# Optimization experiments

Measured on AMD Instinct MI355X. Metric: run time of the kernel, lower is better.

Reference implementation:

```python
import jax, jax.numpy as jnp
import numpy as np
from jax import lax

B, M = 16384, 128
NUM_LAYERS, OW, OH = 22, 11, 11
MAX_VEC = np.array([9.0, 1.0, 1.0, 10.0, 3.0, 254.0, 1.0, 1.0, 235.0, 8.0, 9.0, 250.0,
                    29.0, 1.0, 1.0, 8.0, 1.0, 1.0, 6.0, 3.0, 1.0, 2.0], dtype=np.float32)


def setup_inputs() -> dict:
    key = jax.random.key(0)
    ks = jax.random.split(key, 20)
    s = 0.05
    return {
        "observations": jax.random.randint(ks[0], (B, M, 3), 0, 255, dtype=jnp.int32),
        "cnn1_w": jax.random.normal(ks[1], (64, 22, 5, 5), jnp.float32) * s,
        "cnn1_b": jnp.zeros((64,), jnp.float32),
        "cnn2_w": jax.random.normal(ks[2], (64, 64, 3, 3), jnp.float32) * s,
        "cnn2_b": jnp.zeros((64,), jnp.float32),
        "fc1_w": jax.random.normal(ks[3], (128, 64), jnp.float32) * s,
        "fc1_b": jnp.zeros((128,), jnp.float32),
        "enc_w": jax.random.normal(ks[4], (128, 128), jnp.float32) * s,
        "enc_b": jnp.zeros((128,), jnp.float32),
        "critic1_w": jax.random.normal(ks[5], (1024, 128), jnp.float32) * s,
        "critic1_b": jnp.zeros((1024,), jnp.float32),
        "value_w": jax.random.normal(ks[6], (1, 1024), jnp.float32) * s,
        "value_b": jnp.zeros((1,), jnp.float32),
        "actor1_w": jax.random.normal(ks[7], (512, 128), jnp.float32) * s,
        "actor1_b": jnp.zeros((512,), jnp.float32),
        "action_emb": jax.random.normal(ks[8], (100, 16), jnp.float32) * s,
        "head0_w": jax.random.normal(ks[9], (9, 528), jnp.float32) * s,
        "head0_b": jnp.zeros((9,), jnp.float32),
        "head1_w": jax.random.normal(ks[10], (10, 528), jnp.float32) * s,
        "head1_b": jnp.zeros((10,), jnp.float32),
    }


def _encode_scatter(observations):
    # zero-out any byte equal to 255 (matches torch in-place masking)
    tok = jnp.where(observations == 255, 0, observations)  # [B, M, 3]
    coords = tok[..., 0].astype(jnp.uint8)
    x = ((coords >> 4) & 15).astype(jnp.int32)
    y = (coords & 15).astype(jnp.int32)
    atr = tok[..., 1].astype(jnp.int32)
    val = tok[..., 2].astype(jnp.float32)
    b, m = atr.shape
    valid = (x < OW) & (y < OH) & (atr < NUM_LAYERS)
    b_idx = jnp.broadcast_to(jnp.arange(b, dtype=jnp.int32)[:, None], (b, m))
    b_idx = jnp.where(valid, b_idx, b)  # route invalid tokens out of bounds -> dropped
    box = jnp.zeros((b, NUM_LAYERS, OW, OH), jnp.float32)
    box = box.at[b_idx, atr, x, y].set(val, mode="drop")
    return box


def _forward(observations, cnn1_w, cnn1_b, cnn2_w, cnn2_b, fc1_w, fc1_b, enc_w, enc_b,
             critic1_w, critic1_b, value_w, value_b, actor1_w, actor1_b, action_emb,
             head0_w, head0_b, head1_w, head1_b):
    box = _encode_scatter(observations)
    x = box / jnp.asarray(MAX_VEC)[None, :, None, None]
    dn = ("NCHW", "OIHW", "NCHW")
    x = lax.conv_general_dilated(x, cnn1_w, (3, 3), "VALID", dimension_numbers=dn) + cnn1_b[None, :, None, None]
    x = lax.conv_general_dilated(x, cnn2_w, (1, 1), "VALID", dimension_numbers=dn) + cnn2_b[None, :, None, None]
    x = x.reshape(x.shape[0], -1)                 # [B, 64]
    x = x @ fc1_w.T + fc1_b                       # [B, 128]
    hidden = x @ enc_w.T + enc_b                  # [B, 128]
    critic = jnp.tanh(hidden @ critic1_w.T + critic1_b)
    value = critic @ value_w.T + value_b          # [B, 1]
    actor = hidden @ actor1_w.T + actor1_b        # [B, 512]
    emb = jnp.broadcast_to(action_emb.mean(axis=0)[None, :], (actor.shape[0], action_emb.shape[1]))
    comb = jnp.concatenate([actor, emb], axis=-1)  # [B, 528]
    logits = jnp.concatenate([comb @ head0_w.T + head0_b, comb @ head1_w.T + head1_b], axis=-1)
    return logits, value


def reference(observations, cnn1_w, cnn1_b, cnn2_w, cnn2_b, fc1_w, fc1_b, enc_w, enc_b,
              critic1_w, critic1_b, value_w, value_b, actor1_w, actor1_b, action_emb,
              head0_w, head0_b, head1_w, head1_b):
    return _forward(observations, cnn1_w, cnn1_b, cnn2_w, cnn2_b, fc1_w, fc1_b, enc_w, enc_b,
                    critic1_w, critic1_b, value_w, value_b, actor1_w, actor1_b, action_emb,
                    head0_w, head0_b, head1_w, head1_b)
```

## Files before the change

kernel.cpp:

```cpp
#include <hip/hip_runtime.h>
#include <math.h>

#define NB 16384
#define NTOK 128
#define NKEY 2662
#define NLOG 19
#define TB 16

typedef __attribute__((ext_vector_type(8))) short short8;
typedef __attribute__((ext_vector_type(4))) float floatx4;

__device__ __constant__ float c_maxv[22] = {
    9.f, 1.f, 1.f, 10.f, 3.f, 254.f, 1.f, 1.f, 235.f, 8.f, 9.f, 250.f,
    29.f, 1.f, 1.f, 8.f, 1.f, 1.f, 6.f, 3.f, 1.f, 2.f};

__device__ __forceinline__ unsigned short f2bf(float f) {
    unsigned u = __float_as_uint(f);
    return (unsigned short)((u + 0x7FFFu + ((u >> 16) & 1u)) >> 16);
}
__device__ __forceinline__ float tanh_fast(float x) {
    float e = __builtin_amdgcn_exp2f(x * 2.885390082f);
    return 1.f - 2.f * __builtin_amdgcn_rcpf(e + 1.f);
}

__global__ __launch_bounds__(256) void k_pre1(
    const float* __restrict__ w1, const float* __restrict__ b1,
    const float* __restrict__ w2, const float* __restrict__ b2,
    const float* __restrict__ fc1w, const float* __restrict__ encw,
    const float* __restrict__ h0w, const float* __restrict__ h1w,
    const float* __restrict__ a1w, const float* __restrict__ aemb,
    const float* __restrict__ c1w,
    float* __restrict__ G, float* __restrict__ E,
    float* __restrict__ h2b, float* __restrict__ emb,
    float* __restrict__ Wlog, unsigned short* __restrict__ c1wb)
{
    __shared__ float s_w2[72 * 65];
    const int bid = blockIdx.x, t = threadIdx.x;
    if (bid < 666) {
        const int v = t & 63;
        const int key_u = __builtin_amdgcn_readfirstlane(bid * 4 + (t >> 6));
        const int key_c = (key_u < NKEY) ? key_u : (NKEY - 1);
        const int c = key_c / 121, rem = key_c % 121, X = rem / 11, Y = rem % 11;
        float acc = 0.f;
        for (int u0 = 0; u0 < 64; u0 += 8) {
            __syncthreads();
            #pragma unroll
            for (int r = 0; r < 18; ++r) {
                int g = t + 256 * r;
                int vg = g / 72, rg = g % 72;
                s_w2[rg * 65 + vg] = w2[vg * 576 + u0 * 9 + rg];
            }
            __syncthreads();
            #pragma unroll
            for (int ur = 0; ur < 8; ++ur) {
                const int w1base = (u0 + ur) * 550 + c * 25;
                #pragma unroll
                for (int i = 0; i < 3; ++i) {
                    int xi = X - 3 * i;
                    if (xi < 0 || xi > 4) continue;
                    #pragma unroll
                    for (int j = 0; j < 3; ++j) {
                        int yj = Y - 3 * j;
                        if (yj < 0 || yj > 4) continue;
                        acc += s_w2[(ur * 9 + i * 3 + j) * 65 + v] *
                               w1[w1base + xi * 5 + yj];
                    }
                }
            }
        }
        if (key_u < NKEY) G[key_u * 64 + v] = acc;
    } else if (bid < 698) {
        int m = (bid - 666) * 256 + t;
        int h = __builtin_amdgcn_readfirstlane(m >> 6) & 127;
        int v = t & 63;
        float acc = 0.f;
        #pragma unroll 8
        for (int p = 0; p < 128; ++p)
            acc += encw[h * 128 + p] * fc1w[p * 64 + v];
        E[v * 128 + h] = acc;
    } else if (bid == 698) {
        if (t < 64) {
            float s = b2[t];
            for (int u = 0; u < 64; ++u) {
                float ws = 0.f;
                for (int k = 0; k < 9; ++k) ws += w2[(t * 64 + u) * 9 + k];
                s += b1[u] * ws;
            }
            h2b[t] = s;
        } else if (t < 80) {
            int e = t - 64;
            float s = 0.f;
            for (int r = 0; r < 100; ++r) s += aemb[r * 16 + e];
            emb[e] = s * 0.01f;
        }
    } else if (bid < 709) {
        int n = (bid - 699) * 256 + t;
        if (n < NLOG * 128) {
            int o = __builtin_amdgcn_readfirstlane(n >> 7);
            int h = n & 127;
            const float* hw = (o < 9) ? (h0w + o * 528) : (h1w + (o - 9) * 528);
            float acc = 0.f;
            #pragma unroll 8
            for (int a = 0; a < 512; ++a)
                acc += hw[a] * a1w[a * 128 + h];
            Wlog[n] = acc;
        }
    } else {
        int n = (bid - 709) * 256 + t;
        c1wb[n] = f2bf(c1w[n]);
    }
}

__global__ __launch_bounds__(256) void k_pre2(
    const float* __restrict__ G, const float* __restrict__ E,
    const float* __restrict__ h2b, const float* __restrict__ emb,
    const float* __restrict__ fc1w, const float* __restrict__ fc1b,
    const float* __restrict__ encw, const float* __restrict__ encb,
    const float* __restrict__ a1b,
    const float* __restrict__ h0w, const float* __restrict__ h0b,
    const float* __restrict__ h1w, const float* __restrict__ h1b,
    float* __restrict__ Weff, float* __restrict__ beff, float* __restrict__ blog)
{
    const int bid = blockIdx.x, t = threadIdx.x;
    if (bid < 1331) {
        int n = bid * 256 + t;
        int key = __builtin_amdgcn_readfirstlane(n >> 7);
        int h = n & 127;
        float acc = 0.f;
        #pragma unroll 8
        for (int v = 0; v < 64; ++v)
            acc += E[v * 128 + h] * G[key * 64 + v];
        Weff[n] = acc / c_maxv[key / 121];
    } else {
        __shared__ float s_t[128];
        if (t < 128) {
            float s = fc1b[t];
            for (int v = 0; v < 64; ++v) s += fc1w[t * 64 + v] * h2b[v];
            s_t[t] = s;
        }
        __syncthreads();
        if (t < 128) {
            float s = encb[t];
            for (int p = 0; p < 128; ++p) s += encw[t * 128 + p] * s_t[p];
            beff[t] = s;
        } else if (t < 128 + NLOG) {
            int o = t - 128;
            float s = (o < 9) ? h0b[o] : h1b[o - 9];
            for (int a = 0; a < 512; ++a) {
                float hw = (o < 9) ? h0w[o * 528 + a] : h1w[(o - 9) * 528 + a];
                s += hw * a1b[a];
            }
            for (int e = 0; e < 16; ++e) {
                float hw = (o < 9) ? h0w[o * 528 + 512 + e] : h1w[(o - 9) * 528 + 512 + e];
                s += hw * emb[e];
            }
            blog[o] = s;
        }
    }
}

__global__ __launch_bounds__(256) void k_main(
    const int* __restrict__ obs,
    const float* __restrict__ Weff, const float* __restrict__ beff,
    const unsigned short* __restrict__ c1wb, const float* __restrict__ c1b,
    const float* __restrict__ vw, const float* __restrict__ vb,
    const float* __restrict__ Wlog, const float* __restrict__ blog,
    float* __restrict__ out)
{
    __shared__ int            s_lst[TB * 32];
    __shared__ float          s_hidden[TB * 128];
    __shared__ unsigned short s_hb[TB * 136];
    __shared__ int            s_cnt[TB];
    __shared__ float          s_val[64];

    const int tid = threadIdx.x, bid = blockIdx.x;
    const int b0 = bid * TB;

    if (tid < TB) s_cnt[tid] = 0;
    __syncthreads();

    {
        const int gtok0 = b0 * NTOK;
        #pragma unroll
        for (int k = 0; k < TB * NTOK / 256; ++k) {
            int tt = tid + 256 * k;
            int gi = (gtok0 + tt) * 3;
            int o0 = obs[gi], o1 = obs[gi + 1], o2 = obs[gi + 2];
            o0 = (o0 == 255) ? 0 : o0;
            o1 = (o1 == 255) ? 0 : o1;
            o2 = (o2 == 255) ? 0 : o2;
            int x = (o0 >> 4) & 15, y = o0 & 15;
            if (x < 11 && y < 11 && o1 < 22) {
                int bb = tt >> 7, m = tt & 127;
                int pos = atomicAdd(&s_cnt[bb], 1);
                if (pos < 32)
                    s_lst[bb * 32 + pos] = (m << 20) | (o2 << 12) | (o1 * 121 + x * 11 + y);
            }
        }
    }
    __syncthreads();

    {
        int bb = tid >> 4, e0 = tid & 15;
        int n = s_cnt[bb]; if (n > 32) n = 32;
        #pragma unroll
        for (int r = 0; r < 2; ++r) {
            int e = e0 + 16 * r;
            if (e < n) {
                int p = s_lst[bb * 32 + e];
                bool dead = false;
                for (int i = 0; i < n; ++i) {
                    int q = s_lst[bb * 32 + i];
                    dead |= (((q ^ p) & 0xFFF) == 0) && (q > p);
                }
                if (dead) s_lst[bb * 32 + e] = p & ~0x000FF000;
            }
        }
    }
    __syncthreads();

    {
        int h = tid & 127, bg = tid >> 7;
        for (int bb = bg; bb < TB; bb += 2) {
            float acc = beff[h];
            int n = s_cnt[bb]; if (n > 32) n = 32;
            for (int i = 0; i < n; ++i) {
                int p = s_lst[bb * 32 + i];
                acc += (float)((p >> 12) & 0xFF) * Weff[(p & 0xFFF) * 128 + h];
            }
            s_hidden[bb * 128 + h] = acc;
            s_hb[bb * 136 + h] = f2bf(acc);
        }
    }
    __syncthreads();

    {
        const int lane = tid & 63, w = tid >> 6;
        const int lm = lane & 15, quad = lane >> 4;
        short8 af[4];
        #pragma unroll
        for (int kk = 0; kk < 4; ++kk)
            af[kk] = *(const short8*)&s_hb[lm * 136 + kk * 32 + quad * 8];

        float vpart[4] = {0.f, 0.f, 0.f, 0.f};
        for (int nt = 0; nt < 16; ++nt) {
            int j = w * 256 + nt * 16 + lm;
            floatx4 acc = {0.f, 0.f, 0.f, 0.f};
            #pragma unroll
            for (int kk = 0; kk < 4; ++kk) {
                short8 bf = *(const short8*)&c1wb[j * 128 + kk * 32 + quad * 8];
                acc = __builtin_amdgcn_mfma_f32_16x16x32_bf16(af[kk], bf, acc, 0, 0, 0);
            }
            float bj = c1b[j], wj = vw[j];
            #pragma unroll
            for (int r = 0; r < 4; ++r)
                vpart[r] += tanh_fast(acc[r] + bj) * wj;
        }
        #pragma unroll
        for (int off = 1; off <= 8; off <<= 1)
            #pragma unroll
            for (int r = 0; r < 4; ++r)
                vpart[r] += __shfl_xor(vpart[r], off, 64);
        if (lm == 0) {
            #pragma unroll
            for (int r = 0; r < 4; ++r)
                s_val[w * 16 + quad * 4 + r] = vpart[r];
        }
    }
    __syncthreads();
    if (tid < TB) {
        float v = s_val[tid] + s_val[16 + tid] + s_val[32 + tid] + s_val[48 + tid];
        out[NB * NLOG + b0 + tid] = v + vb[0];
    }

    {
        const float4* s_h4 = (const float4*)s_hidden;
        const float4* wl4  = (const float4*)Wlog;
        int bl = tid >> 4, oo = tid & 15;
        #pragma unroll
        for (int rep = 0; rep < 2; ++rep) {
            int o = oo + rep * 16;
            if (o < NLOG) {
                float acc = blog[o];
                #pragma unroll
                for (int hq = 0; hq < 32; ++hq) {
                    float4 hv = s_h4[bl * 32 + hq];
                    float4 wl = wl4[o * 32 + hq];
                    acc += wl.x * hv.x + wl.y * hv.y + wl.z * hv.z + wl.w * hv.w;
                }
                out[(b0 + bl) * NLOG + o] = acc;
            }
        }
    }
}

extern "C" void kernel_launch(void* const* d_in, const int* in_sizes, int n_in,
                              void* d_out, int out_size, void* d_ws, size_t ws_size,
                              hipStream_t stream)
{
    const int*   obs  = (const int*)  d_in[0];
    const float* w1   = (const float*)d_in[1];
    const float* b1   = (const float*)d_in[2];
    const float* w2   = (const float*)d_in[3];
    const float* b2   = (const float*)d_in[4];
    const float* fc1w = (const float*)d_in[5];
    const float* fc1b = (const float*)d_in[6];
    const float* encw = (const float*)d_in[7];
    const float* encb = (const float*)d_in[8];
    const float* c1w  = (const float*)d_in[9];
    const float* c1b  = (const float*)d_in[10];
    const float* vw   = (const float*)d_in[11];
    const float* vb   = (const float*)d_in[12];
    const float* a1w  = (const float*)d_in[13];
    const float* a1b  = (const float*)d_in[14];
    const float* aemb = (const float*)d_in[15];
    const float* h0w  = (const float*)d_in[16];
    const float* h0b  = (const float*)d_in[17];
    const float* h1w  = (const float*)d_in[18];
    const float* h1b  = (const float*)d_in[19];

    float* W    = (float*)d_ws;
    float* G    = W;
    float* E    = W + 170368;
    float* h2b  = W + 178560;
    float* emb  = W + 178624;
    float* Weff = W + 178640;
    float* beff = W + 519376;
    float* Wlog = W + 519504;
    float* blog = W + 521936;
    unsigned short* c1wb = (unsigned short*)(W + 524288);

    hipLaunchKernelGGL(k_pre1, dim3(1221), dim3(256), 0, stream,
                       w1, b1, w2, b2, fc1w, encw, h0w, h1w, a1w, aemb, c1w,
                       G, E, h2b, emb, Wlog, c1wb);
    hipLaunchKernelGGL(k_pre2, dim3(1332), dim3(256), 0, stream,
                       G, E, h2b, emb, fc1w, fc1b, encw, encb, a1b,
                       h0w, h0b, h1w, h1b, Weff, beff, blog);
    hipLaunchKernelGGL(k_main, dim3(NB / TB), dim3(256), 0, stream,
                       obs, Weff, beff, c1wb, c1b, vw, vb, Wlog, blog,
                       (float*)d_out);
}
```

Before: 210.3 us.

## Double main-kernel batch tile, vectorize loads, and restructure precompute reductions

The main kernel now handles 32 samples per block with 512 threads. Each c1 weight fragment is reused for two MFMA row tiles, observations are read as int4 vectors, and the gather loop for two samples is interleaved to raise memory-level parallelism. The precompute kernels prefetch w2 into registers ahead of the shared-memory store, change the E layout to allow float4 dot products, and split serial reductions (h2b, emb, blog) across threads with shuffles. These changes touch several independent parts and increase per-thread register pressure in exchange for fewer blocks and less redundant weight traffic.

```diff
diff --git a/kernel.cpp b/kernel.cpp
--- a/kernel.cpp
+++ b/kernel.cpp
@@ -5,7 +5,7 @@
 #define NTOK 128
 #define NKEY 2662
 #define NLOG 19
-#define TB 16
+#define TB 32
 
 typedef __attribute__((ext_vector_type(8))) short short8;
 typedef __attribute__((ext_vector_type(4))) float floatx4;
@@ -41,16 +41,43 @@
         const int key_u = __builtin_amdgcn_readfirstlane(bid * 4 + (t >> 6));
         const int key_c = (key_u < NKEY) ? key_u : (NKEY - 1);
         const int c = key_c / 121, rem = key_c % 121, X = rem / 11, Y = rem % 11;
+
+        const int vg0 = t / 72, rg0 = t - vg0 * 72;
+        const int base0 = vg0 * 576 + rg0;
+
+        float rw[18];
+        {
+            int rg = rg0, base = base0;
+            #pragma unroll
+            for (int r = 0; r < 18; ++r) {
+                rw[r] = w2[base];
+                rg += 40; base += 1768;
+                if (rg >= 72) { rg -= 72; base += 504; }
+            }
+        }
         float acc = 0.f;
-        for (int u0 = 0; u0 < 64; u0 += 8) {
+        for (int s = 0; s < 8; ++s) {
             __syncthreads();
-            #pragma unroll
-            for (int r = 0; r < 18; ++r) {
-                int g = t + 256 * r;
-                int vg = g / 72, rg = g % 72;
-                s_w2[rg * 65 + vg] = w2[vg * 576 + u0 * 9 + rg];
+            {
+                int rg = rg0, vg = vg0;
+                #pragma unroll
+                for (int r = 0; r < 18; ++r) {
+                    s_w2[rg * 65 + vg] = rw[r];
+                    rg += 40; vg += 3;
+                    if (rg >= 72) { rg -= 72; vg += 1; }
+                }
             }
             __syncthreads();
+            if (s < 7) {
+                int rg = rg0, base = base0 + (s + 1) * 72;
+                #pragma unroll
+                for (int r = 0; r < 18; ++r) {
+                    rw[r] = w2[base];
+                    rg += 40; base += 1768;
+                    if (rg >= 72) { rg -= 72; base += 504; }
+                }
+            }
+            const int u0 = s * 8;
             #pragma unroll
             for (int ur = 0; ur < 8; ++ur) {
                 const int w1base = (u0 + ur) * 550 + c * 25;
@@ -77,24 +104,33 @@
         #pragma unroll 8
         for (int p = 0; p < 128; ++p)
             acc += encw[h * 128 + p] * fc1w[p * 64 + v];
-        E[v * 128 + h] = acc;
+        E[h * 64 + v] = acc;
     } else if (bid == 698) {
+        int o = t >> 2, q = t & 3;
+        const float* wp = w2 + (o * 64 + q * 16) * 9;
+        float s = 0.f;
+        #pragma unroll
+        for (int ui = 0; ui < 16; ++ui) {
+            float ws = 0.f;
+            #pragma unroll
+            for (int k = 0; k < 9; ++k) ws += wp[ui * 9 + k];
+            s += b1[q * 16 + ui] * ws;
+        }
+        s += __shfl_xor(s, 1, 64);
+        s += __shfl_xor(s, 2, 64);
+        if (q == 0) h2b[o] = s + b2[o];
+    } else if (bid == 699) {
         if (t < 64) {
-            float s = b2[t];
-            for (int u = 0; u < 64; ++u) {
-                float ws = 0.f;
-                for (int k = 0; k < 9; ++k) ws += w2[(t * 64 + u) * 9 + k];
-                s += b1[u] * ws;
-            }
-            h2b[t] = s;
-        } else if (t < 80) {
-            int e = t - 64;
+            int e = t & 15, rq = t >> 4;
             float s = 0.f;
-            for (int r = 0; r < 100; ++r) s += aemb[r * 16 + e];
-            emb[e] = s * 0.01f;
-        }
-    } else if (bid < 709) {
-        int n = (bid - 699) * 256 + t;
+            #pragma unroll
+            for (int rr = 0; rr < 25; ++rr) s += aemb[(rq * 25 + rr) * 16 + e];
+            s += __shfl_xor(s, 16, 64);
+            s += __shfl_xor(s, 32, 64);
+            if (t < 16) emb[e] = s * 0.01f;
+        }
+    } else if (bid < 710) {
+        int n = (bid - 700) * 256 + t;
         if (n < NLOG * 128) {
             int o = __builtin_amdgcn_readfirstlane(n >> 7);
             int h = n & 127;
@@ -106,7 +142,7 @@
             Wlog[n] = acc;
         }
     } else {
-        int n = (bid - 709) * 256 + t;
+        int n = (bid - 710) * 256 + t;
         c1wb[n] = f2bf(c1w[n]);
     }
 }
@@ -121,45 +157,73 @@
     const float* __restrict__ h1w, const float* __restrict__ h1b,
     float* __restrict__ Weff, float* __restrict__ beff, float* __restrict__ blog)
 {
+    __shared__ float s_h2[64];
+    __shared__ float s_t[128];
     const int bid = blockIdx.x, t = threadIdx.x;
     if (bid < 1331) {
         int n = bid * 256 + t;
         int key = __builtin_amdgcn_readfirstlane(n >> 7);
         int h = n & 127;
+        const float4* E4 = (const float4*)E;
+        const float4* G4 = (const float4*)(G + key * 64);
         float acc = 0.f;
-        #pragma unroll 8
-        for (int v = 0; v < 64; ++v)
-            acc += E[v * 128 + h] * G[key * 64 + v];
+        #pragma unroll
+        for (int vq = 0; vq < 16; ++vq) {
+            float4 e = E4[h * 16 + vq];
+            float4 g = G4[vq];
+            acc += e.x * g.x + e.y * g.y + e.z * g.z + e.w * g.w;
+        }
         Weff[n] = acc / c_maxv[key / 121];
     } else {
-        __shared__ float s_t[128];
-        if (t < 128) {
-            float s = fc1b[t];
-            for (int v = 0; v < 64; ++v) s += fc1w[t * 64 + v] * h2b[v];
-            s_t[t] = s;
-        }
+        if (t < 64) s_h2[t] = h2b[t];
         __syncthreads();
         if (t < 128) {
+            const float4* f4 = (const float4*)(fc1w + t * 64);
+            float s = fc1b[t];
+            #pragma unroll
+            for (int vq = 0; vq < 16; ++vq) {
+                float4 w = f4[vq];
+                s += w.x * s_h2[vq * 4]     + w.y * s_h2[vq * 4 + 1] +
+                     w.z * s_h2[vq * 4 + 2] + w.w * s_h2[vq * 4 + 3];
+            }
+            s_t[t] = s;
+        } else {
+            int tp = t - 128;
+            int os = tp >> 3, ai = tp & 7;
+            #pragma unroll
+            for (int rep = 0; rep < 2; ++rep) {
+                int o = os + rep * 16;
+                int oc = (o < NLOG) ? o : (NLOG - 1);
+                const float* hw = (oc < 9) ? (h0w + oc * 528)
+                                           : (h1w + (oc - 9) * 528);
+                float s = 0.f;
+                for (int a = ai; a < 528; a += 8) {
+                    float m = (a < 512) ? a1b[a] : emb[a - 512];
+                    s += hw[a] * m;
+                }
+                s += __shfl_xor(s, 1, 64);
+                s += __shfl_xor(s, 2, 64);
+                s += __shfl_xor(s, 4, 64);
+                if (ai == 0 && o < NLOG)
+                    blog[o] = s + ((o < 9) ? h0b[o] : h1b[o - 9]);
+            }
+        }
+        __syncthreads();
+        if (t < 128) {
+            const float4* e4 = (const float4*)(encw + t * 128);
             float s = encb[t];
-            for (int p = 0; p < 128; ++p) s += encw[t * 128 + p] * s_t[p];
+            #pragma unroll
+            for (int pq = 0; pq < 32; ++pq) {
+                float4 w = e4[pq];
+                s += w.x * s_t[pq * 4]     + w.y * s_t[pq * 4 + 1] +
+                     w.z * s_t[pq * 4 + 2] + w.w * s_t[pq * 4 + 3];
+            }
             beff[t] = s;
-        } else if (t < 128 + NLOG) {
-            int o = t - 128;
-            float s = (o < 9) ? h0b[o] : h1b[o - 9];
-            for (int a = 0; a < 512; ++a) {
-                float hw = (o < 9) ? h0w[o * 528 + a] : h1w[(o - 9) * 528 + a];
-                s += hw * a1b[a];
-            }
-            for (int e = 0; e < 16; ++e) {
-                float hw = (o < 9) ? h0w[o * 528 + 512 + e] : h1w[(o - 9) * 528 + 512 + e];
-                s += hw * emb[e];
-            }
-            blog[o] = s;
-        }
-    }
-}
-
-__global__ __launch_bounds__(256) void k_main(
+        }
+    }
+}
+
+__global__ __launch_bounds__(512, 4) void k_main(
     const int* __restrict__ obs,
     const float* __restrict__ Weff, const float* __restrict__ beff,
     const unsigned short* __restrict__ c1wb, const float* __restrict__ c1b,
@@ -171,7 +235,7 @@
     __shared__ float          s_hidden[TB * 128];
     __shared__ unsigned short s_hb[TB * 136];
     __shared__ int            s_cnt[TB];
-    __shared__ float          s_val[64];
+    __shared__ float          s_val[8 * 32];
 
     const int tid = threadIdx.x, bid = blockIdx.x;
     const int b0 = bid * TB;
@@ -182,19 +246,27 @@
     {
         const int gtok0 = b0 * NTOK;
         #pragma unroll
-        for (int k = 0; k < TB * NTOK / 256; ++k) {
-            int tt = tid + 256 * k;
-            int gi = (gtok0 + tt) * 3;
-            int o0 = obs[gi], o1 = obs[gi + 1], o2 = obs[gi + 2];
-            o0 = (o0 == 255) ? 0 : o0;
-            o1 = (o1 == 255) ? 0 : o1;
-            o2 = (o2 == 255) ? 0 : o2;
-            int x = (o0 >> 4) & 15, y = o0 & 15;
-            if (x < 11 && y < 11 && o1 < 22) {
-                int bb = tt >> 7, m = tt & 127;
-                int pos = atomicAdd(&s_cnt[bb], 1);
-                if (pos < 32)
-                    s_lst[bb * 32 + pos] = (m << 20) | (o2 << 12) | (o1 * 121 + x * 11 + y);
+        for (int k = 0; k < TB * NTOK / (512 * 4); ++k) {
+            int g = tid + 512 * k;
+            const int4* p = (const int4*)(obs + (size_t)(gtok0 + 4 * g) * 3);
+            int4 A = p[0], Bv = p[1], Cv = p[2];
+            int d[12] = {A.x, A.y, A.z, A.w, Bv.x, Bv.y, Bv.z, Bv.w,
+                         Cv.x, Cv.y, Cv.z, Cv.w};
+            #pragma unroll
+            for (int s = 0; s < 4; ++s) {
+                int o0 = d[3 * s], o1 = d[3 * s + 1], o2 = d[3 * s + 2];
+                o0 = (o0 == 255) ? 0 : o0;
+                o1 = (o1 == 255) ? 0 : o1;
+                o2 = (o2 == 255) ? 0 : o2;
+                int x = (o0 >> 4) & 15, y = o0 & 15;
+                if (x < 11 && y < 11 && o1 < 22) {
+                    int tt = 4 * g + s;
+                    int bb = tt >> 7, m = tt & 127;
+                    int pos = atomicAdd(&s_cnt[bb], 1);
+                    if (pos < 32)
+                        s_lst[bb * 32 + pos] =
+                            (m << 20) | (o2 << 12) | (o1 * 121 + x * 11 + y);
+                }
             }
         }
     }
@@ -221,15 +293,26 @@
 
     {
         int h = tid & 127, bg = tid >> 7;
-        for (int bb = bg; bb < TB; bb += 2) {
-            float acc = beff[h];
-            int n = s_cnt[bb]; if (n > 32) n = 32;
-            for (int i = 0; i < n; ++i) {
-                int p = s_lst[bb * 32 + i];
-                acc += (float)((p >> 12) & 0xFF) * Weff[(p & 0xFFF) * 128 + h];
-            }
-            s_hidden[bb * 128 + h] = acc;
-            s_hb[bb * 136 + h] = f2bf(acc);
+        float be = beff[h];
+        #pragma unroll
+        for (int it = 0; it < 4; ++it) {
+            int bbA = bg + it * 8, bbB = bbA + 4;
+            int nA = s_cnt[bbA]; if (nA > 32) nA = 32;
+            int nB = s_cnt[bbB]; if (nB > 32) nB = 32;
+            int nm = (nA > nB) ? nA : nB;
+            float aA = be, aB = be;
+            for (int i = 0; i < nm; ++i) {
+                if (i < nA) {
+                    int p = s_lst[bbA * 32 + i];
+                    aA += (float)((p >> 12) & 0xFF) * Weff[(p & 0xFFF) * 128 + h];
+                }
+                if (i < nB) {
+                    int p = s_lst[bbB * 32 + i];
+                    aB += (float)((p >> 12) & 0xFF) * Weff[(p & 0xFFF) * 128 + h];
+                }
+            }
+            s_hidden[bbA * 128 + h] = aA; s_hb[bbA * 136 + h] = f2bf(aA);
+            s_hidden[bbB * 128 + h] = aB; s_hb[bbB * 136 + h] = f2bf(aB);
         }
     }
     __syncthreads();
@@ -237,39 +320,51 @@
     {
         const int lane = tid & 63, w = tid >> 6;
         const int lm = lane & 15, quad = lane >> 4;
-        short8 af[4];
-        #pragma unroll
-        for (int kk = 0; kk < 4; ++kk)
-            af[kk] = *(const short8*)&s_hb[lm * 136 + kk * 32 + quad * 8];
-
-        float vpart[4] = {0.f, 0.f, 0.f, 0.f};
-        for (int nt = 0; nt < 16; ++nt) {
-            int j = w * 256 + nt * 16 + lm;
-            floatx4 acc = {0.f, 0.f, 0.f, 0.f};
+        short8 af0[4], af1[4];
+        #pragma unroll
+        for (int kk = 0; kk < 4; ++kk) {
+            af0[kk] = *(const short8*)&s_hb[lm * 136 + kk * 32 + quad * 8];
+            af1[kk] = *(const short8*)&s_hb[(16 + lm) * 136 + kk * 32 + quad * 8];
+        }
+        float vp0[4] = {0.f, 0.f, 0.f, 0.f}, vp1[4] = {0.f, 0.f, 0.f, 0.f};
+        for (int nt = 0; nt < 8; ++nt) {
+            int j = w * 128 + nt * 16 + lm;
+            const short8* cp = (const short8*)&c1wb[j * 128];
+            floatx4 a0 = {0.f, 0.f, 0.f, 0.f}, a1 = {0.f, 0.f, 0.f, 0.f};
             #pragma unroll
             for (int kk = 0; kk < 4; ++kk) {
-                short8 bf = *(const short8*)&c1wb[j * 128 + kk * 32 + quad * 8];
-                acc = __builtin_amdgcn_mfma_f32_16x16x32_bf16(af[kk], bf, acc, 0, 0, 0);
+                short8 bf = cp[kk * 4 + quad];
+                a0 = __builtin_amdgcn_mfma_f32_16x16x32_bf16(af0[kk], bf, a0, 0, 0, 0);
+                a1 = __builtin_amdgcn_mfma_f32_16x16x32_bf16(af1[kk], bf, a1, 0, 0, 0);
             }
             float bj = c1b[j], wj = vw[j];
             #pragma unroll
-            for (int r = 0; r < 4; ++r)
-                vpart[r] += tanh_fast(acc[r] + bj) * wj;
-        }
-        #pragma unroll
-        for (int off = 1; off <= 8; off <<= 1)
-            #pragma unroll
-            for (int r = 0; r < 4; ++r)
-                vpart[r] += __shfl_xor(vpart[r], off, 64);
+            for (int r = 0; r < 4; ++r) {
+                vp0[r] += tanh_fast(a0[r] + bj) * wj;
+                vp1[r] += tanh_fast(a1[r] + bj) * wj;
+            }
+        }
+        #pragma unroll
+        for (int off = 1; off <= 8; off <<= 1) {
+            #pragma unroll
+            for (int r = 0; r < 4; ++r) {
+                vp0[r] += __shfl_xor(vp0[r], off, 64);
+                vp1[r] += __shfl_xor(vp1[r], off, 64);
+            }
+        }
         if (lm == 0) {
             #pragma unroll
-            for (int r = 0; r < 4; ++r)
-                s_val[w * 16 + quad * 4 + r] = vpart[r];
+            for (int r = 0; r < 4; ++r) {
+                s_val[w * 32 + quad * 4 + r]      = vp0[r];
+                s_val[w * 32 + 16 + quad * 4 + r] = vp1[r];
+            }
         }
     }
     __syncthreads();
     if (tid < TB) {
-        float v = s_val[tid] + s_val[16 + tid] + s_val[32 + tid] + s_val[48 + tid];
+        float v = 0.f;
+        #pragma unroll
+        for (int w = 0; w < 8; ++w) v += s_val[w * 32 + tid];
         out[NB * NLOG + b0 + tid] = v + vb[0];
     }
 
@@ -330,13 +425,13 @@
     float* blog = W + 521936;
     unsigned short* c1wb = (unsigned short*)(W + 524288);
 
-    hipLaunchKernelGGL(k_pre1, dim3(1221), dim3(256), 0, stream,
+    hipLaunchKernelGGL(k_pre1, dim3(1222), dim3(256), 0, stream,
                        w1, b1, w2, b2, fc1w, encw, h0w, h1w, a1w, aemb, c1w,
                        G, E, h2b, emb, Wlog, c1wb);
     hipLaunchKernelGGL(k_pre2, dim3(1332), dim3(256), 0, stream,
                        G, E, h2b, emb, fc1w, fc1b, encw, encb, a1b,
                        h0w, h0b, h1w, h1b, Weff, beff, blog);
-    hipLaunchKernelGGL(k_main, dim3(NB / TB), dim3(256), 0, stream,
+    hipLaunchKernelGGL(k_main, dim3(NB / TB), dim3(512), 0, stream,
                        obs, Weff, beff, c1wb, c1b, vw, vb, Wlog, blog,
                        (float*)d_out);
 }
```

Result: slower. 214.7 us (+2.1%).
